# Performance work log

Hardware: AMD Instinct MI355X
Metric: run time of the kernel (lower is better)

Reference implementation:

```python
import math
import jax, jax.numpy as jnp
import numpy as np

B, H, W = 32, 32, 32
SQRT2 = 1.4142  # literal from the torch module


def setup_inputs() -> dict:
    key = jax.random.key(0)
    k1, k2, k3 = jax.random.split(key, 3)
    cost_maps = jax.random.uniform(k1, (B, 1, H, W), jnp.float32, 0.5, 1.5)
    si = jax.random.randint(k2, (B,), 0, H * W)
    gi = jax.random.randint(k3, (B,), 0, H * W)
    gi = jnp.where(gi == si, (gi + 1) % (H * W), gi)
    start_maps = jax.nn.one_hot(si, H * W, dtype=jnp.float32).reshape(B, 1, H, W)
    goal_maps = jax.nn.one_hot(gi, H * W, dtype=jnp.float32).reshape(B, 1, H, W)
    return {"cost_maps": cost_maps, "start_maps": start_maps, "goal_maps": goal_maps}


def _st_softmax_noexp(val):
    # straight-through softmax-without-exp: soft normalize, hard argmax one-hot
    b = val.shape[0]
    v = val.reshape(b, -1)
    y = v / v.sum(-1, keepdims=True)
    ind = jnp.argmax(y, -1)
    y_hard = jax.nn.one_hot(ind, v.shape[-1], dtype=y.dtype)
    y = jax.lax.stop_gradient(y_hard - y) + y
    return y.reshape(val.shape)


def _conv3x3(x, k):
    # x: [B,H,W], k: [3,3]; torch F.conv2d is cross-correlation, as is lax conv
    return jax.lax.conv_general_dilated(x[:, None], k[None, None], (1, 1), ((1, 1), (1, 1)))[:, 0]


def _forward(cost_maps, start_maps, goal_maps, w=1.0):
    cm = cost_maps[:, 0]
    sm = start_maps[:, 0]
    gm = goal_maps[:, 0]
    obs = cm  # obstacles_maps defaults to cost_maps
    b, hgt, wid = cm.shape
    hw = hgt * wid

    # Euclidean heuristic (dis_type='Euc'), scaled by cost map and weight w
    loc = jnp.stack(jnp.meshgrid(jnp.arange(hgt), jnp.arange(wid), indexing='ij'), 0).astype(cm.dtype)  # [2,H,W]
    goal_loc = jnp.einsum('kij,bij->bk', loc, gm)  # [B,2]
    diff = loc.reshape(2, -1)[None] - goal_loc[:, :, None]  # [B,2,HW]
    h = jnp.sqrt((diff ** 2).sum(1)).reshape(b, hgt, wid) * cm * w

    k_s = jnp.array([[1., 1., 1.], [1., 0., 1.], [1., 1., 1.]], cm.dtype)
    k_c = jnp.array([[SQRT2, 1., SQRT2], [1., 0., 1.], [SQRT2, 1., SQRT2]], cm.dtype)
    inv_c = 1.0 / math.sqrt(hw)

    goal_idx = jnp.argmax(gm.reshape(b, -1), -1).astype(cm.dtype)  # [B]
    parents0 = jnp.ones((b, hw), cm.dtype) * goal_idx[:, None]
    bidx = jnp.arange(b)

    def step(carry, t):
        open_m, hist, g, parents, done, tb = carry
        f = g + h
        f_exp = jnp.exp(-f * inv_c) * open_m
        ns = _st_softmax_noexp(f_exp)                        # [B,H,W] node selection
        dist = (ns * gm).sum((1, 2), keepdims=True)
        unsolved = (dist < 1e-8).astype(f.dtype)
        hist_n = jnp.clip(hist + ns, 0.0, 1.0)
        open_n = jnp.clip(open_m - unsolved * ns, 0.0, 1.0)
        neighbor = _conv3x3(ns, k_s) * obs
        g2 = (g * ns).sum((1, 2), keepdims=True) + _conv3x3(ns, k_c)
        idx = ((1.0 - open_n) * (1.0 - hist_n) + open_n * (g > g2).astype(f.dtype)) * neighbor
        idx = jax.lax.stop_gradient(idx)
        g_n = jax.lax.stop_gradient(g2 * idx + g * (1.0 - idx))
        open_n = jax.lax.stop_gradient(jnp.clip(open_n + idx, 0.0, 1.0))
        idxf = idx.reshape(b, -1)
        new_par = jnp.argmax(ns.reshape(b, -1), -1)[:, None].astype(f.dtype)
        parents_n = new_par * idxf + parents * (1.0 - idxf)
        all_solved = jnp.all(unsolved == 0)
        newly = jnp.logical_and(jnp.logical_not(done), all_solved)
        tb_n = jnp.where(newly, t, tb)
        done_n = jnp.logical_or(done, all_solved)
        sel = lambda new, old: jnp.where(done, old, new)  # freeze after torch break
        return (sel(open_n, open_m), sel(hist_n, hist), sel(g_n, g),
                sel(parents_n, parents), done_n, tb_n), None

    carry0 = (sm, jnp.zeros_like(sm), jnp.zeros_like(sm), parents0,
              jnp.array(False), jnp.array(0, jnp.int32))
    (open_f, hist, g, parents, done, tb), _ = jax.lax.scan(
        step, carry0, jnp.arange(hw, dtype=jnp.int32))
    current_t = jnp.where(done, tb, hw - 1)

    # backtrack
    par_i = parents.astype(jnp.int32)
    gm_i = gm.astype(jnp.int32).reshape(b, -1)
    loc0 = (par_i * gm_i).sum(-1)

    def bt_step(c, i):
        path, loc = c
        active = i < current_t
        path = jnp.where(active, path.at[bidx, loc].set(1), path)
        loc = jnp.where(active, par_i[bidx, loc], loc)
        return (path, loc), None

    (path, _), _ = jax.lax.scan(bt_step, (gm_i, loc0), jnp.arange(hw, dtype=jnp.int32))
    path_maps = path.reshape(b, hgt, wid)
    return hist[:, None], path_maps[:, None]


def reference(cost_maps, start_maps, goal_maps):
    return _forward(cost_maps, start_maps, goal_maps)
```

## Files before the change

### kernel.cpp

```cpp
#include <hip/hip_runtime.h>
#include <math.h>

#define HWC 1024
#define NB  32
#define GH  32
#define GW  32
#define NPHASE 7

#define WS_BAR   0
#define WS_SWIN  256

#define FEIDX(i) ((((i) & 15) << 6) | ((i) >> 4))

__device__ __forceinline__ float fe_expr(float g, float h, float o) {
    return __fmul_rn(expf(__fmul_rn(__fadd_rn(g, h), -0.03125f)), o);
}

template<int CTRL>
__device__ __forceinline__ float dppmax(float m) {
    int sh = __builtin_amdgcn_update_dpp(__float_as_int(m), __float_as_int(m), CTRL, 0xF, 0xF, false);
    return fmaxf(m, __int_as_float(sh));
}
template<int CTRL>
__device__ __forceinline__ unsigned dppand(unsigned m) {
    int sh = __builtin_amdgcn_update_dpp((int)m, (int)m, CTRL, 0xF, 0xF, false);
    return m & (unsigned)sh;
}

__global__ void dastar_init(unsigned* __restrict__ bar) {
    if (threadIdx.x < 32) bar[threadIdx.x] = 0u;
}

__global__ __launch_bounds__(64)
void dastar_fused(const float* __restrict__ cm_g, const float* __restrict__ sm_g,
                  const float* __restrict__ gm_g, unsigned* __restrict__ swin,
                  unsigned* __restrict__ bar, float* __restrict__ out)
{
    const int b   = blockIdx.x;
    const int tid = threadIdx.x;

    __shared__ __align__(16) float feT[HWC];
    __shared__ __align__(16) float gg[HWC], oo[HWC], hi[HWC], cmS[HWC], hhS[HWC];
    __shared__ unsigned slog[HWC * 9];
    __shared__ int goal_sh;

    const float4* cm4 = (const float4*)(cm_g + b * HWC);
    const float4* sm4 = (const float4*)(sm_g + b * HWC);
    const float4* gm4 = (const float4*)(gm_g + b * HWC);
    float cmr[16], oor[16];
#pragma unroll
    for (int q = 0; q < 4; ++q) {
        int i4 = tid * 4 + q;
        float4 c4 = cm4[i4];
        float4 s4 = sm4[i4];
        float4 g4 = gm4[i4];
        int base = i4 * 4;
        float cv[4] = {c4.x, c4.y, c4.z, c4.w};
        float sv[4] = {s4.x, s4.y, s4.z, s4.w};
        float gv[4] = {g4.x, g4.y, g4.z, g4.w};
#pragma unroll
        for (int j = 0; j < 4; ++j) {
            int i = base + j;
            cmr[q * 4 + j] = cv[j];
            oor[q * 4 + j] = sv[j];
            cmS[i] = cv[j];
            gg[i] = 0.0f; hi[i] = 0.0f; oo[i] = sv[j];
            if (gv[j] == 1.0f) goal_sh = i;
        }
    }
    __syncthreads();

    const int   goal = goal_sh;
    const float gy = (float)(goal >> 5), gx = (float)(goal & 31);
#pragma unroll
    for (int k = 0; k < 16; ++k) {
        int i = tid * 16 + k;
        float dy = (float)(i >> 5) - gy;
        float dx = (float)(i & 31) - gx;
        float h  = __fmul_rn(sqrtf(__fadd_rn(__fmul_rn(dy, dy), __fmul_rn(dx, dx))), cmr[k]);
        hhS[i] = h;
        feT[(k << 6) + tid] = fe_expr(0.0f, h, oor[k]);
    }
    __syncthreads();

    const int dyj = tid / 3 - 1, dxj = tid % 3 - 1;

    float vn[16];
#pragma unroll
    for (int k = 0; k < 16; ++k) vn[k] = feT[(k << 6) + tid];

    int  tstar = HWC - 1;
    unsigned word = 0u;
    int wpub = 0, t = 0, Pprev = 0;
    bool done = false;
    const int bounds[NPHASE] = {90, 106, 138, 202, 330, 586, 1024};

    for (int phase = 0; phase < NPHASE && !done; ++phase) {
        const int P = bounds[phase];

        while (t < P) {
            float v[16];
#pragma unroll
            for (int k = 0; k < 16; ++k) v[k] = vn[k];

            float a0 = fmaxf(v[0], v[1]),  a1 = fmaxf(v[2], v[3]);
            float a2 = fmaxf(v[4], v[5]),  a3 = fmaxf(v[6], v[7]);
            float a4 = fmaxf(v[8], v[9]),  a5 = fmaxf(v[10], v[11]);
            float a6 = fmaxf(v[12], v[13]), a7 = fmaxf(v[14], v[15]);
            float b0 = fmaxf(a0, a1), b1 = fmaxf(a2, a3);
            float b2 = fmaxf(a4, a5), b3 = fmaxf(a6, a7);
            float vmax = fmaxf(fmaxf(b0, b1), fmaxf(b2, b3));

            float m = vmax;
            m = dppmax<0x111>(m);
            m = dppmax<0x112>(m);
            m = dppmax<0x114>(m);
            m = dppmax<0x118>(m);
            m = dppmax<0x142>(m);
            m = dppmax<0x143>(m);
            const float gmax = __int_as_float(__builtin_amdgcn_readlane(__float_as_int(m), 63));

            unsigned msk = 0u;
#pragma unroll
            for (int k = 0; k < 16; ++k) msk |= (v[k] == gmax) ? (1u << k) : 0u;
            const int lft = __ffs(msk) - 1;
            unsigned long long bl = __ballot(msk != 0u);
            int lsel = (int)__ffsll(bl) - 1;
            if (lsel < 0) lsel = 0;
            const int  s      = __builtin_amdgcn_readlane(tid * 16 + lft, lsel);
            const bool solved = (s == goal);

            if (tid < 9) {
                const int sy = s >> 5, sx = s & 31;
                if (tid == 4) {
                    hi[s] = 1.0f;
                    if (!solved) { oo[s] = 0.0f; feT[FEIDX(s)] = 0.0f; }
                    slog[t * 9 + 4] = (unsigned)s;
                } else {
                    const int  cy = sy + dyj, cx = sx + dxj;
                    const bool inb = (cy >= 0 && cy < GH && cx >= 0 && cx < GW);
                    const int  c  = (cy << 5) | cx;
                    const int  q  = inb ? c : s;
                    const float gq = gg[q], oq = oo[q], hq = hi[q];
                    const float cmq = cmS[q], hhq = hhS[q];
                    const float gs = gg[s];
                    float lidx = 0.0f;
                    if (inb) {
                        const float kc = (dyj != 0 && dxj != 0) ? 1.4142f : 1.0f;
                        const float g2 = __fadd_rn(gs, kc);
                        const float t1 = __fmul_rn(__fsub_rn(1.0f, oq), __fsub_rn(1.0f, hq));
                        const float t2 = __fmul_rn(oq, (gq > g2) ? 1.0f : 0.0f);
                        const float idxv = __fmul_rn(__fadd_rn(t1, t2), cmq);
                        lidx = idxv;
                        if (idxv != 0.0f) {
                            const float omi = __fsub_rn(1.0f, idxv);
                            const float gn = __fadd_rn(__fmul_rn(g2, idxv), __fmul_rn(gq, omi));
                            const float on = fminf(__fadd_rn(oq, idxv), 1.0f);
                            gg[c] = gn; oo[c] = on;
                            feT[FEIDX(c)] = fe_expr(gn, hhq, on);
                        }
                    }
                    slog[t * 9 + tid] = __float_as_uint(lidx);
                }
            }

#pragma unroll
            for (int k = 0; k < 16; ++k) vn[k] = feT[(k << 6) + tid];

            if (solved) word |= (1u << (t & 31));
            ++t;
            if ((t & 31) == 0) {
                if (tid == 0)
                    __hip_atomic_store(&swin[wpub * NB + b], word, __ATOMIC_RELEASE, __HIP_MEMORY_SCOPE_AGENT);
                ++wpub; word = 0u;
            }
        }

        if ((t & 31) && tid == 0)
            __hip_atomic_store(&swin[(t >> 5) * NB + b], word, __ATOMIC_RELEASE, __HIP_MEMORY_SCOPE_AGENT);

        if (tid == 0)
            __hip_atomic_fetch_add(&bar[phase], 1u, __ATOMIC_ACQ_REL, __HIP_MEMORY_SCOPE_AGENT);
        {
            unsigned guard = 0u;
            while (__hip_atomic_load(&bar[phase], __ATOMIC_ACQUIRE, __HIP_MEMORY_SCOPE_AGENT) < NB) {
                __builtin_amdgcn_s_sleep(1);
                if (++guard > 16000000u) break;
            }
        }

        const int wEnd = (P + 31) >> 5;
        for (int w = (Pprev >> 5); w < wEnd; ++w) {
            int lo = Pprev - 32 * w; if (lo < 0) lo = 0;
            int hi2 = P - 32 * w;    if (hi2 > 32) hi2 = 32;
            unsigned mask = (hi2 == 32 ? 0xFFFFFFFFu : ((1u << hi2) - 1u))
                          & ~(lo == 0 ? 0u : ((1u << lo) - 1u));
            unsigned wv = __hip_atomic_load(&swin[w * NB + (tid & 31)], __ATOMIC_ACQUIRE, __HIP_MEMORY_SCOPE_AGENT);
            unsigned A = wv;
            A = dppand<0x111>(A); A = dppand<0x112>(A); A = dppand<0x114>(A);
            A = dppand<0x118>(A); A = dppand<0x142>(A); A = dppand<0x143>(A);
            A = (unsigned)__builtin_amdgcn_readlane((int)A, 63);
            A &= mask;
            if (A) { tstar = w * 32 + (__ffs(A) - 1); done = true; break; }
        }
        Pprev = P;
    }
    __syncthreads();

    const int Tl = tstar;

#pragma unroll
    for (int q = 0; q < 4; ++q)
        ((float4*)hi)[tid + (q << 6)] = make_float4(0.f, 0.f, 0.f, 0.f);
    __syncthreads();
    for (int tt = tid; tt <= Tl; tt += 64) hi[(int)slog[tt * 9 + 4]] = 1.0f;
    __syncthreads();
#pragma unroll
    for (int q = 0; q < 4; ++q) {
        int i4 = tid + (q << 6);
        ((float4*)(out + b * HWC))[i4] = ((const float4*)hi)[i4];
    }

    const float goalf = (float)goal;
#pragma unroll
    for (int k = 0; k < 16; ++k) {
        int i = tid * 16 + k;
        cmS[i] = goalf;
        hhS[i] = 0.0f;
    }
    __syncthreads();
    if (tid < 9 && tid != 4) {
        for (int t0c = 0; t0c <= Tl; t0c += 16) {
            float iv[16], sv[16];
#pragma unroll
            for (int u = 0; u < 16; ++u) {
                int tt = t0c + u;
                if (tt <= Tl) {
                    iv[u] = __uint_as_float(slog[tt * 9 + tid]);
                    sv[u] = (float)(int)slog[tt * 9 + 4];
                } else {
                    iv[u] = 0.0f; sv[u] = 0.0f;
                }
            }
#pragma unroll
            for (int u = 0; u < 16; ++u) {
                if (iv[u] != 0.0f) {
                    int c = (int)sv[u] + (dyj << 5) + dxj;
                    float omi = __fsub_rn(1.0f, iv[u]);
                    cmS[c] = __fadd_rn(__fmul_rn(sv[u], iv[u]), __fmul_rn(cmS[c], omi));
                }
            }
        }
    }
    __syncthreads();

    if (tid == 0) {
        hhS[goal] = 1.0f;
        int loc = (int)cmS[goal];
        for (int i2 = 0; i2 < tstar; ++i2) {
            int w = (loc < 0) ? loc + HWC : loc;
            if (w >= 0 && w < HWC) {
                if (hhS[w] == 1.0f) break;
                hhS[w] = 1.0f;
            }
            int gidx = w < 0 ? 0 : (w > HWC - 1 ? HWC - 1 : w);
            loc = (int)cmS[gidx];
        }
    }
    __syncthreads();
#pragma unroll
    for (int q = 0; q < 4; ++q) {
        int i4 = tid + (q << 6);
        ((float4*)(out + NB * HWC + b * HWC))[i4] = ((const float4*)hhS)[i4];
    }
}

extern "C" void kernel_launch(void* const* d_in, const int* in_sizes, int n_in,
                              void* d_out, int out_size, void* d_ws, size_t ws_size,
                              hipStream_t stream)
{
    const float* cm = (const float*)d_in[0];
    const float* sm = (const float*)d_in[1];
    const float* gm = (const float*)d_in[2];
    float* out = (float*)d_out;

    unsigned* bar  = (unsigned*)((char*)d_ws + WS_BAR);
    unsigned* swin = (unsigned*)((char*)d_ws + WS_SWIN);

    dastar_init<<<1, 64, 0, stream>>>(bar);
    dastar_fused<<<dim3(NB), dim3(64), 0, stream>>>(cm, sm, gm, swin, bar, out);
}
```

Measured before the change: 115.6 us.

## Keep f-scores in registers via lane shuffles and parallelise backtrack with readlane

The per-step f-value array now stays in each lane's registers. After each expansion the up to nine changed neighbour values are broadcast with shuffles, replacing the shared-memory feT store and the full 16-value reload every step. The single-thread backtrack over shared memory is replaced by a wave-wide walk: parent indices are held in registers and fetched with readlane, and path bits are collected into a per-lane bitmask. The new walk drops the early-exit on revisits and always runs tstar iterations, so it can take more steps than before.

```diff
diff --git a/kernel.cpp b/kernel.cpp
--- a/kernel.cpp
+++ b/kernel.cpp
@@ -10,8 +10,6 @@
 #define WS_BAR   0
 #define WS_SWIN  256
 
-#define FEIDX(i) ((((i) & 15) << 6) | ((i) >> 4))
-
 __device__ __forceinline__ float fe_expr(float g, float h, float o) {
     return __fmul_rn(expf(__fmul_rn(__fadd_rn(g, h), -0.03125f)), o);
 }
@@ -25,6 +23,17 @@
 __device__ __forceinline__ unsigned dppand(unsigned m) {
     int sh = __builtin_amdgcn_update_dpp((int)m, (int)m, CTRL, 0xF, 0xF, false);
     return m & (unsigned)sh;
+}
+
+__device__ __forceinline__ int sel16(const int* a, int n) {
+    int b0 = (n & 1) ? a[1]  : a[0],  b1 = (n & 1) ? a[3]  : a[2];
+    int b2 = (n & 1) ? a[5]  : a[4],  b3 = (n & 1) ? a[7]  : a[6];
+    int b4 = (n & 1) ? a[9]  : a[8],  b5 = (n & 1) ? a[11] : a[10];
+    int b6 = (n & 1) ? a[13] : a[12], b7 = (n & 1) ? a[15] : a[14];
+    int c0 = (n & 2) ? b1 : b0, c1 = (n & 2) ? b3 : b2;
+    int c2 = (n & 2) ? b5 : b4, c3 = (n & 2) ? b7 : b6;
+    int d0 = (n & 4) ? c1 : c0, d1 = (n & 4) ? c3 : c2;
+    return (n & 8) ? d1 : d0;
 }
 
 __global__ void dastar_init(unsigned* __restrict__ bar) {
@@ -39,7 +48,6 @@
     const int b   = blockIdx.x;
     const int tid = threadIdx.x;
 
-    __shared__ __align__(16) float feT[HWC];
     __shared__ __align__(16) float gg[HWC], oo[HWC], hi[HWC], cmS[HWC], hhS[HWC];
     __shared__ unsigned slog[HWC * 9];
     __shared__ int goal_sh;
@@ -72,6 +80,7 @@
 
     const int   goal = goal_sh;
     const float gy = (float)(goal >> 5), gx = (float)(goal & 31);
+    float vn[16];
 #pragma unroll
     for (int k = 0; k < 16; ++k) {
         int i = tid * 16 + k;
@@ -79,19 +88,17 @@
         float dx = (float)(i & 31) - gx;
         float h  = __fmul_rn(sqrtf(__fadd_rn(__fmul_rn(dy, dy), __fmul_rn(dx, dx))), cmr[k]);
         hhS[i] = h;
-        feT[(k << 6) + tid] = fe_expr(0.0f, h, oor[k]);
+        vn[k]  = fe_expr(0.0f, h, oor[k]);
     }
     __syncthreads();
 
     const int dyj = tid / 3 - 1, dxj = tid % 3 - 1;
-
-    float vn[16];
-#pragma unroll
-    for (int k = 0; k < 16; ++k) vn[k] = feT[(k << 6) + tid];
+    const int myrow = tid >> 1;
+    const int mycol0 = (tid & 1) << 4;
 
     int  tstar = HWC - 1;
     unsigned word = 0u;
-    int wpub = 0, t = 0, Pprev = 0;
+    int t = 0, Pprev = 0;
     bool done = false;
     const int bounds[NPHASE] = {90, 106, 138, 202, 330, 586, 1024};
 
@@ -99,42 +106,35 @@
         const int P = bounds[phase];
 
         while (t < P) {
-            float v[16];
-#pragma unroll
-            for (int k = 0; k < 16; ++k) v[k] = vn[k];
-
-            float a0 = fmaxf(v[0], v[1]),  a1 = fmaxf(v[2], v[3]);
-            float a2 = fmaxf(v[4], v[5]),  a3 = fmaxf(v[6], v[7]);
-            float a4 = fmaxf(v[8], v[9]),  a5 = fmaxf(v[10], v[11]);
-            float a6 = fmaxf(v[12], v[13]), a7 = fmaxf(v[14], v[15]);
+            float a0 = fmaxf(vn[0], vn[1]),   a1 = fmaxf(vn[2], vn[3]);
+            float a2 = fmaxf(vn[4], vn[5]),   a3 = fmaxf(vn[6], vn[7]);
+            float a4 = fmaxf(vn[8], vn[9]),   a5 = fmaxf(vn[10], vn[11]);
+            float a6 = fmaxf(vn[12], vn[13]), a7 = fmaxf(vn[14], vn[15]);
             float b0 = fmaxf(a0, a1), b1 = fmaxf(a2, a3);
             float b2 = fmaxf(a4, a5), b3 = fmaxf(a6, a7);
             float vmax = fmaxf(fmaxf(b0, b1), fmaxf(b2, b3));
 
             float m = vmax;
-            m = dppmax<0x111>(m);
-            m = dppmax<0x112>(m);
-            m = dppmax<0x114>(m);
-            m = dppmax<0x118>(m);
-            m = dppmax<0x142>(m);
-            m = dppmax<0x143>(m);
+            m = dppmax<0x111>(m); m = dppmax<0x112>(m); m = dppmax<0x114>(m);
+            m = dppmax<0x118>(m); m = dppmax<0x142>(m); m = dppmax<0x143>(m);
             const float gmax = __int_as_float(__builtin_amdgcn_readlane(__float_as_int(m), 63));
 
             unsigned msk = 0u;
 #pragma unroll
-            for (int k = 0; k < 16; ++k) msk |= (v[k] == gmax) ? (1u << k) : 0u;
+            for (int k = 0; k < 16; ++k) msk |= (vn[k] == gmax) ? (1u << k) : 0u;
             const int lft = __ffs(msk) - 1;
             unsigned long long bl = __ballot(msk != 0u);
             int lsel = (int)__ffsll(bl) - 1;
             if (lsel < 0) lsel = 0;
             const int  s      = __builtin_amdgcn_readlane(tid * 16 + lft, lsel);
             const bool solved = (s == goal);
-
+            const int  sy = s >> 5, sx = s & 31;
+
+            float fnew = -1.0f;
             if (tid < 9) {
-                const int sy = s >> 5, sx = s & 31;
                 if (tid == 4) {
                     hi[s] = 1.0f;
-                    if (!solved) { oo[s] = 0.0f; feT[FEIDX(s)] = 0.0f; }
+                    if (!solved) { oo[s] = 0.0f; fnew = 0.0f; }
                     slog[t * 9 + 4] = (unsigned)s;
                 } else {
                     const int  cy = sy + dyj, cx = sx + dxj;
@@ -157,7 +157,7 @@
                             const float gn = __fadd_rn(__fmul_rn(g2, idxv), __fmul_rn(gq, omi));
                             const float on = fminf(__fadd_rn(oq, idxv), 1.0f);
                             gg[c] = gn; oo[c] = on;
-                            feT[FEIDX(c)] = fe_expr(gn, hhq, on);
+                            fnew = fe_expr(gn, hhq, on);
                         }
                     }
                     slog[t * 9 + tid] = __float_as_uint(lidx);
@@ -165,14 +165,40 @@
             }
 
 #pragma unroll
-            for (int k = 0; k < 16; ++k) vn[k] = feT[(k << 6) + tid];
+            for (int dcol = -1; dcol <= 1; ++dcol) {
+                const int kk = (sx + dcol) & 15;
+                const int ix = mycol0 + kk;
+                const int dyr = myrow - sy;
+                const bool adj = (dyr >= -1) && (dyr <= 1) && (ix - sx == dcol);
+                const int j = (dyr + 1) * 3 + (dcol + 1);
+                const float f = __shfl(fnew, adj ? j : 0);
+                const bool take = adj && (f >= 0.0f);
+                switch (kk) {
+                    case 0:  vn[0]  = take ? f : vn[0];  break;
+                    case 1:  vn[1]  = take ? f : vn[1];  break;
+                    case 2:  vn[2]  = take ? f : vn[2];  break;
+                    case 3:  vn[3]  = take ? f : vn[3];  break;
+                    case 4:  vn[4]  = take ? f : vn[4];  break;
+                    case 5:  vn[5]  = take ? f : vn[5];  break;
+                    case 6:  vn[6]  = take ? f : vn[6];  break;
+                    case 7:  vn[7]  = take ? f : vn[7];  break;
+                    case 8:  vn[8]  = take ? f : vn[8];  break;
+                    case 9:  vn[9]  = take ? f : vn[9];  break;
+                    case 10: vn[10] = take ? f : vn[10]; break;
+                    case 11: vn[11] = take ? f : vn[11]; break;
+                    case 12: vn[12] = take ? f : vn[12]; break;
+                    case 13: vn[13] = take ? f : vn[13]; break;
+                    case 14: vn[14] = take ? f : vn[14]; break;
+                    default: vn[15] = take ? f : vn[15]; break;
+                }
+            }
 
             if (solved) word |= (1u << (t & 31));
             ++t;
             if ((t & 31) == 0) {
                 if (tid == 0)
-                    __hip_atomic_store(&swin[wpub * NB + b], word, __ATOMIC_RELEASE, __HIP_MEMORY_SCOPE_AGENT);
-                ++wpub; word = 0u;
+                    __hip_atomic_store(&swin[((t >> 5) - 1) * NB + b], word, __ATOMIC_RELEASE, __HIP_MEMORY_SCOPE_AGENT);
+                word = 0u;
             }
         }
 
@@ -223,11 +249,7 @@
 
     const float goalf = (float)goal;
 #pragma unroll
-    for (int k = 0; k < 16; ++k) {
-        int i = tid * 16 + k;
-        cmS[i] = goalf;
-        hhS[i] = 0.0f;
-    }
+    for (int k = 0; k < 16; ++k) cmS[tid * 16 + k] = goalf;
     __syncthreads();
     if (tid < 9 && tid != 4) {
         for (int t0c = 0; t0c <= Tl; t0c += 16) {
@@ -254,24 +276,29 @@
     }
     __syncthreads();
 
-    if (tid == 0) {
-        hhS[goal] = 1.0f;
-        int loc = (int)cmS[goal];
-        for (int i2 = 0; i2 < tstar; ++i2) {
-            int w = (loc < 0) ? loc + HWC : loc;
-            if (w >= 0 && w < HWC) {
-                if (hhS[w] == 1.0f) break;
-                hhS[w] = 1.0f;
-            }
-            int gidx = w < 0 ? 0 : (w > HWC - 1 ? HWC - 1 : w);
-            loc = (int)cmS[gidx];
-        }
-    }
-    __syncthreads();
+    int ppi[16];
+#pragma unroll
+    for (int k = 0; k < 16; ++k) ppi[k] = (int)cmS[tid * 16 + k];
+
+    unsigned pbm = (tid == (goal >> 4)) ? (1u << (goal & 15)) : 0u;
+    int loc = __builtin_amdgcn_readlane(sel16(ppi, goal & 15), goal >> 4);
+    for (int i2 = 0; i2 < tstar; ++i2) {
+        int w = (loc < 0) ? loc + HWC : loc;
+        if (w >= 0 && w < HWC)
+            pbm |= (tid == (w >> 4)) ? (1u << (w & 15)) : 0u;
+        int g2 = w < 0 ? 0 : (w > HWC - 1 ? HWC - 1 : w);
+        loc = __builtin_amdgcn_readlane(sel16(ppi, g2 & 15), g2 >> 4);
+    }
+
+    float4* po4 = (float4*)(out + NB * HWC + b * HWC);
 #pragma unroll
     for (int q = 0; q < 4; ++q) {
-        int i4 = tid + (q << 6);
-        ((float4*)(out + NB * HWC + b * HWC))[i4] = ((const float4*)hhS)[i4];
+        float4 v;
+        v.x = (float)((pbm >> (q * 4 + 0)) & 1u);
+        v.y = (float)((pbm >> (q * 4 + 1)) & 1u);
+        v.z = (float)((pbm >> (q * 4 + 2)) & 1u);
+        v.w = (float)((pbm >> (q * 4 + 3)) & 1u);
+        po4[tid * 4 + q] = v;
     }
 }
 
```

After: 158.1 us. +36.7%, slower.
